# Optimization experiments

Measured on AMD Instinct MI355X. Metric: run time of the kernel, lower is better.

The kernel has to match this reference:

```python
import jax, jax.numpy as jnp
import numpy as np
import math

# ---- static config (mirrors init_kwargs) ----
B, CIN, COUT = 8, 32, 32
H, W = 256, 256
RADIUS_CUTOFF = 0.03
NR, NPHI = 6, 7               # kernel_shape = [6, 7] (anisotropic basis)
K = (NR - 1) * NPHI + 1       # 36 basis functions
EPS = 1e-5                    # InstanceNorm2d eps
NEG_SLOPE = 0.2


def _disco_psi(nh, nw, r_cutoff, nr, nphi):
    """Local DISCO filter basis on an equidistant [-1,1]^2 grid.
    Returns psi [K, P, P] (float32) and half-width p (P = 2p+1).
    Piecewise-linear hat functions in radius (nr rings incl. center) times
    hat functions in angle (nphi sectors), normalized and quadrature-weighted."""
    dy = 2.0 / nh
    dx = 2.0 / nw
    p = int(math.floor(r_cutoff / min(dx, dy)))
    off_y = (np.arange(-p, p + 1) * dy)[:, None]
    off_x = (np.arange(-p, p + 1) * dx)[None, :]
    r = np.sqrt(off_x ** 2 + off_y ** 2)                 # [P, P]
    phi = np.arctan2(off_y + 0 * off_x, off_x + 0 * off_y) % (2.0 * np.pi)
    dr = r_cutoff / nr
    dphi = 2.0 * np.pi / nphi
    ker = (nr - 1) * nphi + 1
    ik = np.arange(ker)[:, None, None]                   # [K,1,1]
    ir = ((ik - 1) // nphi + 1) * dr                     # ik=0 -> ring at r=0
    iphi = ((ik - 1) % nphi) * dphi
    norm = np.pi * (r_cutoff * nr / (nr + 1)) ** 2       # 2d normalization
    rv = np.clip(1.0 - np.abs(r[None] - ir) / dr, 0.0, None) * (r[None] <= r_cutoff)
    dphi_abs = np.abs(phi[None] - iphi)
    dphi_min = np.minimum(dphi_abs, 2.0 * np.pi - dphi_abs)
    pv = np.where(ik > 0, np.clip(1.0 - dphi_min / dphi, 0.0, None), 1.0)
    q = dx * dy                                          # quadrature weight
    psi = (rv * pv) * (q / norm)
    return jnp.asarray(psi, jnp.float32), p


def _upsample2x_bilinear_align_corners(x):
    """torch nn.Upsample(scale_factor=2, mode='bilinear', align_corners=True)."""
    b, c, hi, wi = x.shape
    ho, wo = 2 * hi, 2 * wi
    ys = jnp.linspace(0.0, hi - 1.0, ho)
    y0 = jnp.clip(jnp.floor(ys), 0, hi - 2).astype(jnp.int32)
    wy = (ys - y0.astype(ys.dtype))[None, None, :, None]
    x = x[:, :, y0, :] * (1.0 - wy) + x[:, :, y0 + 1, :] * wy
    xs = jnp.linspace(0.0, wi - 1.0, wo)
    x0 = jnp.clip(jnp.floor(xs), 0, wi - 2).astype(jnp.int32)
    wx = (xs - x0.astype(xs.dtype))[None, None, None, :]
    return x[:, :, :, x0] * (1.0 - wx) + x[:, :, :, x0 + 1] * wx


def setup_inputs() -> dict:
    key = jax.random.key(0)
    k1, k2 = jax.random.split(key)
    image = jax.random.normal(k1, (B, CIN, H, W), dtype=jnp.float32)
    # DISCO learnable weights: [out_ch, in_ch, kernel_size]
    scale = 1.0 / np.sqrt(CIN * K)
    weight = jax.random.normal(k2, (COUT, CIN, K), dtype=jnp.float32) * scale
    return {"image": image, "weight": weight}


def reference(image, weight):
    x = _upsample2x_bilinear_align_corners(image)
    # 2) equidistant DISCO conv: assemble dense kernel from basis, strided conv back to (H,W)
    psi, p = _disco_psi(2 * H, 2 * W, RADIUS_CUTOFF / 2.0, NR, NPHI)   # [K,P,P]
    kernel = jnp.einsum("oik,kyx->oiyx", weight, psi)                   # [O,I,P,P]
    y = jax.lax.conv_general_dilated(
        x, kernel, window_strides=(2, 2), padding=[(p, p), (p, p)],
        dimension_numbers=("NCHW", "OIHW", "NCHW"))                     # [B,O,H,W]
    # 3) InstanceNorm2d (no affine), biased variance over spatial dims
    mean = jnp.mean(y, axis=(2, 3), keepdims=True)
    var = jnp.var(y, axis=(2, 3), keepdims=True)
    y = (y - mean) * jax.lax.rsqrt(var + EPS)
    # 4) LeakyReLU(0.2)
    return jnp.where(y >= 0, y, NEG_SLOPE * y)
```

## Files before the change

kernel.cpp:

```cpp
#include <hip/hip_runtime.h>
#include <hip/hip_bf16.h>
#include <math.h>

#define B_     8
#define CIN_   32
#define COUT_  32
#define H_     256
#define W_     256
#define K_     36
#define P_     3
#define KW_    7
#define TAPS_  49
#define EPS_   1e-5f
#define SLOPE_ 0.2f
#define ISTEP_ (255.0f / 511.0f)

#define PART_OFF_F  25600

#define IMG_PLANE_B   6400
#define IMG_ROW_B     320

using short8_t  = __attribute__((ext_vector_type(8)))  short;
using f32x16_t  = __attribute__((ext_vector_type(16))) float;
using f32x4_t   = __attribute__((ext_vector_type(4)))  float;

#define SWZ(a) ((a) ^ ((((a) >> 7) & 1) << 4))

__device__ inline ushort f32_to_bf16(float f) {
    unsigned int bits = __float_as_uint(f);
    unsigned int r = (bits + 0x7FFFu + ((bits >> 16) & 1u)) >> 16;
    return (ushort)r;
}

__global__ __launch_bounds__(256)
void build_kernel(const float* __restrict__ weight, ushort* __restrict__ kerB) {
    __shared__ float psi_s[K_];
    const int tap = blockIdx.x;
    const int ty  = tap / KW_;
    const int tx  = tap % KW_;
    const int tid = threadIdx.x;

    if (tid < K_) {
        const double dxy   = 2.0 / 512.0;
        const double rcut  = 0.015;
        const int    nr    = 6, nphi = 7;
        const double dr    = rcut / nr;
        const double dphi  = 2.0 * M_PI / nphi;
        const double norm  = M_PI * (rcut * nr / (nr + 1)) * (rcut * nr / (nr + 1));
        const double q     = dxy * dxy;

        const double offy = (double)(ty - P_) * dxy;
        const double offx = (double)(tx - P_) * dxy;
        const double r    = sqrt(offx * offx + offy * offy);
        double phi = atan2(offy, offx);
        if (phi < 0.0) phi += 2.0 * M_PI;

        const int k = tid;
        double ir, iphi;
        if (k == 0) { ir = 0.0; iphi = 0.0; }
        else        { ir = (double)((k - 1) / nphi + 1) * dr;
                      iphi = (double)((k - 1) % nphi) * dphi; }

        double rv = 1.0 - fabs(r - ir) / dr;
        rv = rv > 0.0 ? rv : 0.0;
        if (r > rcut) rv = 0.0;

        double pv = 1.0;
        if (k > 0) {
            double da = fabs(phi - iphi);
            double dm = da < (2.0 * M_PI - da) ? da : (2.0 * M_PI - da);
            pv = 1.0 - dm / dphi;
            pv = pv > 0.0 ? pv : 0.0;
        }
        psi_s[k] = (float)(rv * pv * q / norm);
    }
    __syncthreads();

    for (int e = tid; e < 1024; e += 256) {
        const int g16  = e >> 9;
        const int lane = (e >> 3) & 63;
        const int j    = e & 7;
        const int o    = lane & 31;
        const int ci   = g16 * 16 + ((lane >> 5) & 1) * 8 + j;
        const float* w = weight + (size_t)(o * CIN_ + ci) * K_;
        float s = 0.f;
        #pragma unroll
        for (int k = 0; k < K_; ++k) s = fmaf(w[k], psi_s[k], s);
        kerB[((size_t)(g16 * 49 + tap) * 64 + lane) * 8 + j] = f32_to_bf16(s);
    }
}

__global__ __launch_bounds__(512, 4)
void conv_mfma(const float* __restrict__ image,
               const ushort* __restrict__ kerB,
               float* __restrict__ out,
               float* __restrict__ partials) {
    __shared__ float  Img_s[6400];
    __shared__ ushort Xup_s[2738 * 8];
    __shared__ int    ryt[37];  __shared__ float wyt[37];
    __shared__ int    rxt[37];  __shared__ float wxt[37];
    __shared__ float  wp[8][32][2];

    const int tid  = threadIdx.x;
    const int lane = tid & 63;
    const int w    = tid >> 6;
    const int j0 = blockIdx.x * 16;
    const int i0 = blockIdx.y * 16;
    const int b  = blockIdx.z;

    const int u0 = 2 * i0 - 3;
    const int v0 = 2 * j0 - 3;
    const int u_min = u0 > 0 ? u0 : 0;
    const int v_min = v0 > 0 ? v0 : 0;
    int r0 = (int)floorf((float)u_min * ISTEP_); if (r0 > 254) r0 = 254;
    int c0 = (int)floorf((float)v_min * ISTEP_); if (c0 > 254) c0 = 254;

    if (tid < 37) {
        const int u = u0 + tid;
        const float ysf = (float)u * ISTEP_;
        int yy0 = (int)ysf; yy0 = yy0 < 0 ? 0 : (yy0 > 254 ? 254 : yy0);
        int ry = yy0 - r0; ry = ry < 0 ? 0 : (ry > 18 ? 18 : ry);
        ryt[tid] = ry;
        wyt[tid] = ysf - (float)yy0;
    } else if (tid >= 64 && tid < 101) {
        const int x = tid - 64;
        const int v = v0 + x;
        const float xsf = (float)v * ISTEP_;
        int xx0 = (int)xsf; xx0 = xx0 < 0 ? 0 : (xx0 > 254 ? 254 : xx0);
        int rx = xx0 - c0; rx = rx < 0 ? 0 : (rx > 18 ? 18 : rx);
        rxt[x] = rx;
        wxt[x] = xsf - (float)xx0;
    }

    const int gs  = lane >> 5;
    const int tio = (lane & 31) >> 4;
    const int tj  = lane & 15;
    const int yb0 = 4 * w + 2 * tio;
    const int xb  = 2 * tj;

    f32x16_t acc;
    #pragma unroll
    for (int q = 0; q < 16; ++q) acc[q] = 0.f;

    char* img_bytes = (char*)Img_s;
    char* xup_bytes = (char*)Xup_s;

    for (int g16 = 0; g16 < 2; ++g16) {
        const float* img = image + (size_t)(b * CIN_ + g16 * 16) * (H_ * W_);
        for (int e = tid; e < 1600; e += 512) {
            const int p  = e / 400;
            const int yx = e - p * 400;
            const int py = yx / 20, px = yx - py * 20;
            const int row = r0 + py, col = c0 + px;
            f32x4_t g = {0.f, 0.f, 0.f, 0.f};
            if (row < H_ && col < W_) {
                const float* q = img + (size_t)p * 4 * (H_ * W_) + row * W_ + col;
                g[0] = q[0];
                g[1] = q[H_ * W_];
                g[2] = q[2 * H_ * W_];
                g[3] = q[3 * H_ * W_];
            }
            *(f32x4_t*)(img_bytes + p * IMG_PLANE_B + yx * 16) = g;
        }
        __syncthreads();

        for (int e = tid; e < 1369; e += 512) {
            const int y = e / 37;
            const int x = e - y * 37;
            const int ry = ryt[y]; const float wy = wyt[y];
            const int rx = rxt[x]; const float wx = wxt[x];
            const bool ok = ((unsigned)(u0 + y) < 512u) && ((unsigned)(v0 + x) < 512u);
            const int cbase = (ry * 20 + rx) * 16;
            #pragma unroll
            for (int gsub = 0; gsub < 2; ++gsub) {
                const char* lo = img_bytes + gsub * (2 * IMG_PLANE_B) + cbase;
                const char* hi = lo + IMG_PLANE_B;
                const f32x4_t a00 = *(const f32x4_t*)(lo);
                const f32x4_t a01 = *(const f32x4_t*)(lo + 16);
                const f32x4_t a10 = *(const f32x4_t*)(lo + IMG_ROW_B);
                const f32x4_t a11 = *(const f32x4_t*)(lo + IMG_ROW_B + 16);
                const f32x4_t b00 = *(const f32x4_t*)(hi);
                const f32x4_t b01 = *(const f32x4_t*)(hi + 16);
                const f32x4_t b10 = *(const f32x4_t*)(hi + IMG_ROW_B);
                const f32x4_t b11 = *(const f32x4_t*)(hi + IMG_ROW_B + 16);
                f32x4_t t0 = a00 + wx * (a01 - a00);
                f32x4_t t1 = a10 + wx * (a11 - a10);
                f32x4_t lo4 = t0 + wy * (t1 - t0);
                t0 = b00 + wx * (b01 - b00);
                t1 = b10 + wx * (b11 - b10);
                f32x4_t hi4 = t0 + wy * (t1 - t0);
                __hip_bfloat162 h0 = __float22bfloat162_rn(make_float2(lo4[0], lo4[1]));
                __hip_bfloat162 h1 = __float22bfloat162_rn(make_float2(lo4[2], lo4[3]));
                __hip_bfloat162 h2 = __float22bfloat162_rn(make_float2(hi4[0], hi4[1]));
                __hip_bfloat162 h3 = __float22bfloat162_rn(make_float2(hi4[2], hi4[3]));
                union { short8_t s8; uint4 u4; } pk;
                pk.u4.x = ok ? *(unsigned int*)&h0 : 0u;
                pk.u4.y = ok ? *(unsigned int*)&h1 : 0u;
                pk.u4.z = ok ? *(unsigned int*)&h2 : 0u;
                pk.u4.w = ok ? *(unsigned int*)&h3 : 0u;
                const int addr = SWZ((e + gsub * 1369) << 4);
                *(short8_t*)(xup_bytes + addr) = pk.s8;
            }
        }
        __syncthreads();

        const ushort* kbp = kerB + ((size_t)(g16 * 49 * 64 + lane)) * 8;
        #pragma unroll
        for (int ky = 0; ky < KW_; ++ky) {
            short8_t bf[KW_];
            #pragma unroll
            for (int kx = 0; kx < KW_; ++kx)
                bf[kx] = *(const short8_t*)(kbp + (size_t)(ky * KW_ + kx) * 512);
            const int rowbase = (gs * 1369 + (yb0 + ky) * 37 + xb) << 4;
            #pragma unroll
            for (int kx = 0; kx < KW_; ++kx) {
                const int a0 = SWZ(rowbase + (kx << 4));
                const short8_t afrag = *(const short8_t*)(xup_bytes + a0);
                acc = __builtin_amdgcn_mfma_f32_32x32x16_bf16(afrag, bf[kx], acc, 0, 0, 0);
            }
        }
        __syncthreads();
    }

    const int n = lane & 31;
    float* op = out + (size_t)(b * COUT_ + n) * (H_ * W_);
    const int ibase = i0 + 2 * w;
    #pragma unroll
    for (int grp = 0; grp < 4; ++grp) {
        const int ti  = ibase + (grp >> 1);
        const int tjj = j0 + ((grp & 1) ? 8 : 0) + 4 * gs;
        f32x4_t s;
        s[0] = acc[grp * 4 + 0]; s[1] = acc[grp * 4 + 1];
        s[2] = acc[grp * 4 + 2]; s[3] = acc[grp * 4 + 3];
        *(f32x4_t*)(op + (size_t)ti * W_ + tjj) = s;
    }

    float s1 = 0.f, s2 = 0.f;
    #pragma unroll
    for (int q = 0; q < 16; ++q) { s1 += acc[q]; s2 = fmaf(acc[q], acc[q], s2); }
    s1 += __shfl_xor(s1, 32);
    s2 += __shfl_xor(s2, 32);
    if (lane < 32) { wp[w][lane][0] = s1; wp[w][lane][1] = s2; }
    __syncthreads();
    if (tid < 32) {
        float t1 = 0.f, t2 = 0.f;
        #pragma unroll
        for (int wv = 0; wv < 8; ++wv) { t1 += wp[wv][tid][0]; t2 += wp[wv][tid][1]; }
        const int tile = blockIdx.y * 16 + blockIdx.x;
        float2* pp = (float2*)partials;
        pp[((b * 32 + tid) << 8) | tile] = make_float2(t1, t2);
    }
}

__global__ __launch_bounds__(256)
void norm2_kernel(float* __restrict__ y, const float* __restrict__ partials) {
    __shared__ float r1[256];
    __shared__ float r2[256];
    const int tid = threadIdx.x;
    const int blk = blockIdx.x;
    const int bo  = blk >> 6;
    const float2 p = ((const float2*)partials)[(bo << 8) | tid];
    r1[tid] = p.x; r2[tid] = p.y;
    __syncthreads();
    for (int off = 128; off > 0; off >>= 1) {
        if (tid < off) { r1[tid] += r1[tid + off]; r2[tid] += r2[tid + off]; }
        __syncthreads();
    }
    const float inv = 1.0f / 65536.0f;
    const float m   = r1[0] * inv;
    const float var = r2[0] * inv - m * m;
    const float rs  = 1.0f / sqrtf(var + EPS_);

    const int e = blk * 256 + tid;
    float4 v = ((const float4*)y)[e];
    v.x = (v.x - m) * rs; v.x = v.x >= 0.f ? v.x : SLOPE_ * v.x;
    v.y = (v.y - m) * rs; v.y = v.y >= 0.f ? v.y : SLOPE_ * v.y;
    v.z = (v.z - m) * rs; v.z = v.z >= 0.f ? v.z : SLOPE_ * v.z;
    v.w = (v.w - m) * rs; v.w = v.w >= 0.f ? v.w : SLOPE_ * v.w;
    ((float4*)y)[e] = v;
}

extern "C" void kernel_launch(void* const* d_in, const int* in_sizes, int n_in,
                              void* d_out, int out_size, void* d_ws, size_t ws_size,
                              hipStream_t stream) {
    const float* image  = (const float*)d_in[0];
    const float* weight = (const float*)d_in[1];
    float*  out      = (float*)d_out;
    ushort* kerB     = (ushort*)d_ws;
    float*  partials = (float*)d_ws + PART_OFF_F;

    build_kernel<<<dim3(TAPS_), dim3(256), 0, stream>>>(weight, kerB);
    conv_mfma<<<dim3(16, 16, B_), dim3(512), 0, stream>>>(image, kerB, out, partials);
    norm2_kernel<<<dim3(16384), dim3(256), 0, stream>>>(out, partials);
}
```

Baseline: 130.6 us.

## Use closed-form bilinear upsample weights and separable per-thread row/column interpolation

```diff
diff --git a/kernel.cpp b/kernel.cpp
--- a/kernel.cpp
+++ b/kernel.cpp
@@ -13,12 +13,11 @@
 #define TAPS_  49
 #define EPS_   1e-5f
 #define SLOPE_ 0.2f
-#define ISTEP_ (255.0f / 511.0f)
 
 #define PART_OFF_F  25600
 
-#define IMG_PLANE_B   6400
-#define IMG_ROW_B     320
+#define IMG_PLANE_B   6736
+#define IMG_ROW_B     336
 
 using short8_t  = __attribute__((ext_vector_type(8)))  short;
 using f32x16_t  = __attribute__((ext_vector_type(16))) float;
@@ -95,10 +94,8 @@
                const ushort* __restrict__ kerB,
                float* __restrict__ out,
                float* __restrict__ partials) {
-    __shared__ float  Img_s[6400];
+    __shared__ float  Img_s[6736];
     __shared__ ushort Xup_s[2738 * 8];
-    __shared__ int    ryt[37];  __shared__ float wyt[37];
-    __shared__ int    rxt[37];  __shared__ float wxt[37];
     __shared__ float  wp[8][32][2];
 
     const int tid  = threadIdx.x;
@@ -110,27 +107,8 @@
 
     const int u0 = 2 * i0 - 3;
     const int v0 = 2 * j0 - 3;
-    const int u_min = u0 > 0 ? u0 : 0;
-    const int v_min = v0 > 0 ? v0 : 0;
-    int r0 = (int)floorf((float)u_min * ISTEP_); if (r0 > 254) r0 = 254;
-    int c0 = (int)floorf((float)v_min * ISTEP_); if (c0 > 254) c0 = 254;
-
-    if (tid < 37) {
-        const int u = u0 + tid;
-        const float ysf = (float)u * ISTEP_;
-        int yy0 = (int)ysf; yy0 = yy0 < 0 ? 0 : (yy0 > 254 ? 254 : yy0);
-        int ry = yy0 - r0; ry = ry < 0 ? 0 : (ry > 18 ? 18 : ry);
-        ryt[tid] = ry;
-        wyt[tid] = ysf - (float)yy0;
-    } else if (tid >= 64 && tid < 101) {
-        const int x = tid - 64;
-        const int v = v0 + x;
-        const float xsf = (float)v * ISTEP_;
-        int xx0 = (int)xsf; xx0 = xx0 < 0 ? 0 : (xx0 > 254 ? 254 : xx0);
-        int rx = xx0 - c0; rx = rx < 0 ? 0 : (rx > 18 ? 18 : rx);
-        rxt[x] = rx;
-        wxt[x] = xsf - (float)xx0;
-    }
+    const int R0 = i0 - 2;
+    const int C0 = j0 - 2;
 
     const int gs  = lane >> 5;
     const int tio = (lane & 31) >> 4;
@@ -151,55 +129,68 @@
             const int p  = e / 400;
             const int yx = e - p * 400;
             const int py = yx / 20, px = yx - py * 20;
-            const int row = r0 + py, col = c0 + px;
+            const int row = R0 + py, col = C0 + px;
             f32x4_t g = {0.f, 0.f, 0.f, 0.f};
-            if (row < H_ && col < W_) {
+            if ((unsigned)row < 256u && (unsigned)col < 256u) {
                 const float* q = img + (size_t)p * 4 * (H_ * W_) + row * W_ + col;
                 g[0] = q[0];
                 g[1] = q[H_ * W_];
                 g[2] = q[2 * H_ * W_];
                 g[3] = q[3 * H_ * W_];
             }
-            *(f32x4_t*)(img_bytes + p * IMG_PLANE_B + yx * 16) = g;
-        }
-        __syncthreads();
-
-        for (int e = tid; e < 1369; e += 512) {
-            const int y = e / 37;
-            const int x = e - y * 37;
-            const int ry = ryt[y]; const float wy = wyt[y];
-            const int rx = rxt[x]; const float wx = wxt[x];
-            const bool ok = ((unsigned)(u0 + y) < 512u) && ((unsigned)(v0 + x) < 512u);
-            const int cbase = (ry * 20 + rx) * 16;
-            #pragma unroll
-            for (int gsub = 0; gsub < 2; ++gsub) {
-                const char* lo = img_bytes + gsub * (2 * IMG_PLANE_B) + cbase;
-                const char* hi = lo + IMG_PLANE_B;
-                const f32x4_t a00 = *(const f32x4_t*)(lo);
-                const f32x4_t a01 = *(const f32x4_t*)(lo + 16);
-                const f32x4_t a10 = *(const f32x4_t*)(lo + IMG_ROW_B);
-                const f32x4_t a11 = *(const f32x4_t*)(lo + IMG_ROW_B + 16);
-                const f32x4_t b00 = *(const f32x4_t*)(hi);
-                const f32x4_t b01 = *(const f32x4_t*)(hi + 16);
-                const f32x4_t b10 = *(const f32x4_t*)(hi + IMG_ROW_B);
-                const f32x4_t b11 = *(const f32x4_t*)(hi + IMG_ROW_B + 16);
-                f32x4_t t0 = a00 + wx * (a01 - a00);
-                f32x4_t t1 = a10 + wx * (a11 - a10);
-                f32x4_t lo4 = t0 + wy * (t1 - t0);
-                t0 = b00 + wx * (b01 - b00);
-                t1 = b10 + wx * (b11 - b10);
-                f32x4_t hi4 = t0 + wy * (t1 - t0);
-                __hip_bfloat162 h0 = __float22bfloat162_rn(make_float2(lo4[0], lo4[1]));
-                __hip_bfloat162 h1 = __float22bfloat162_rn(make_float2(lo4[2], lo4[3]));
-                __hip_bfloat162 h2 = __float22bfloat162_rn(make_float2(hi4[0], hi4[1]));
-                __hip_bfloat162 h3 = __float22bfloat162_rn(make_float2(hi4[2], hi4[3]));
-                union { short8_t s8; uint4 u4; } pk;
-                pk.u4.x = ok ? *(unsigned int*)&h0 : 0u;
-                pk.u4.y = ok ? *(unsigned int*)&h1 : 0u;
-                pk.u4.z = ok ? *(unsigned int*)&h2 : 0u;
-                pk.u4.w = ok ? *(unsigned int*)&h3 : 0u;
-                const int addr = SWZ((e + gsub * 1369) << 4);
-                *(short8_t*)(xup_bytes + addr) = pk.s8;
+            *(f32x4_t*)(img_bytes + p * IMG_PLANE_B + (py * 21 + px) * 16) = g;
+        }
+        __syncthreads();
+
+        for (int e = tid; e < 518; e += 512) {
+            const int g   = (e >= 259) ? 1 : 0;
+            const int r   = e - 259 * g;
+            const int y   = r / 7;
+            const int c   = r - 7 * y;
+            const int x0  = 6 * c;
+            const int ry  = y >> 1;
+            const int Ay  = R0 + ry;
+            const float wy = (float)(((y & 1) ? 510 : 255) - Ay) * (1.0f / 511.0f);
+            const bool oky = ((unsigned)(u0 + y) < 512u);
+
+            const char* lo = img_bytes + (2 * g) * IMG_PLANE_B
+                           + (ry * 21 + (x0 >> 1)) * 16;
+            const char* hi = lo + IMG_PLANE_B;
+            f32x4_t colA[4], colB[4];
+            #pragma unroll
+            for (int k = 0; k < 4; ++k) {
+                const f32x4_t a0 = *(const f32x4_t*)(lo + k * 16);
+                const f32x4_t a1 = *(const f32x4_t*)(lo + k * 16 + IMG_ROW_B);
+                colA[k] = a0 + wy * (a1 - a0);
+                const f32x4_t b0 = *(const f32x4_t*)(hi + k * 16);
+                const f32x4_t b1 = *(const f32x4_t*)(hi + k * 16 + IMG_ROW_B);
+                colB[k] = b0 + wy * (b1 - b0);
+            }
+
+            const int base_idx = g * 1369 + y * 37;
+            #pragma unroll
+            for (int m = 0; m < 6; ++m) {
+                const int x = x0 + m;
+                if (x < 37) {
+                    const int cx = m >> 1;
+                    const int Ax = C0 + (x >> 1);
+                    const float wx =
+                        (float)(((x & 1) ? 510 : 255) - Ax) * (1.0f / 511.0f);
+                    const f32x4_t va = colA[cx] + wx * (colA[cx + 1] - colA[cx]);
+                    const f32x4_t vb = colB[cx] + wx * (colB[cx + 1] - colB[cx]);
+                    const bool ok = oky && ((unsigned)(v0 + x) < 512u);
+                    __hip_bfloat162 h0 = __float22bfloat162_rn(make_float2(va[0], va[1]));
+                    __hip_bfloat162 h1 = __float22bfloat162_rn(make_float2(va[2], va[3]));
+                    __hip_bfloat162 h2 = __float22bfloat162_rn(make_float2(vb[0], vb[1]));
+                    __hip_bfloat162 h3 = __float22bfloat162_rn(make_float2(vb[2], vb[3]));
+                    union { short8_t s8; uint4 u4; } pk;
+                    pk.u4.x = ok ? *(unsigned int*)&h0 : 0u;
+                    pk.u4.y = ok ? *(unsigned int*)&h1 : 0u;
+                    pk.u4.z = ok ? *(unsigned int*)&h2 : 0u;
+                    pk.u4.w = ok ? *(unsigned int*)&h3 : 0u;
+                    const int addr = SWZ((base_idx + x) << 4);
+                    *(short8_t*)(xup_bytes + addr) = pk.s8;
+                }
             }
         }
         __syncthreads();
```

Result: slower. 157.0 us (+20.2%).
